# Kernel tuning notes

Hardware: AMD Instinct MI355X
Metric: run time of the kernel (lower is better)

The kernel has to match this reference:

```python
import jax, jax.numpy as jnp
import numpy as np

B, S, D, H = 2, 2048, 1024, 16
DK = D // H


def setup_inputs() -> dict:
    key = jax.random.key(0)
    ks = jax.random.split(key, 12)
    s = 1.0 / np.sqrt(D)
    return {
        "query": jax.random.normal(ks[0], (B, S, D), dtype=jnp.float32),
        "key": jax.random.normal(ks[1], (B, S, D), dtype=jnp.float32),
        "value": jax.random.normal(ks[2], (B, S, D), dtype=jnp.float32),
        "mask": jax.random.randint(ks[3], (B, 1, 1, S), 0, 2, dtype=jnp.int32),
        "wq": jax.random.normal(ks[4], (D, D), dtype=jnp.float32) * s,
        "bq": jnp.zeros((D,), dtype=jnp.float32),
        "wk": jax.random.normal(ks[5], (D, D), dtype=jnp.float32) * s,
        "bk": jnp.zeros((D,), dtype=jnp.float32),
        "wv": jax.random.normal(ks[6], (D, D), dtype=jnp.float32) * s,
        "bv": jnp.zeros((D,), dtype=jnp.float32),
        "wo": jax.random.normal(ks[7], (D, D), dtype=jnp.float32) * s,
        "bo": jnp.zeros((D,), dtype=jnp.float32),
    }


def reference(query, key, value, mask, wq, bq, wk, bk, wv, bv, wo, bo):
    b, s, d = query.shape
    # torch Linear: y = x @ W^T + b, then split heads -> [B, H, S, dk]
    def proj(x, w, bias):
        return (x @ w.T + bias).reshape(b, -1, H, DK).transpose(0, 2, 1, 3)

    q = proj(query, wq, bq)
    k = proj(key, wk, bk)
    v = proj(value, wv, bv)

    scores = jnp.einsum("bhqd,bhkd->bhqk", q, k) / jnp.sqrt(jnp.float32(DK))
    scores = jnp.where(mask == 0, jnp.float32(-1e9), scores)
    attn = jax.nn.softmax(scores, axis=-1)  # [B,H,S,S]
    x = jnp.einsum("bhqk,bhkd->bhqd", attn, v)
    x = x.transpose(0, 2, 1, 3).reshape(b, s, d)
    return x @ wo.T + bo
```

## Files before the change

kernel.cpp:

```cpp
#include <hip/hip_runtime.h>
#include <math.h>

#define B_  2
#define S_  2048
#define D_  1024
#define H_  16
#define DK_ 64
#define NT_ (S_ / 64)

typedef unsigned short u16;
typedef unsigned int u32;
typedef __bf16 bf16x8 __attribute__((ext_vector_type(8)));
typedef float f32x4 __attribute__((ext_vector_type(4)));

typedef const __attribute__((address_space(1))) void* gas1_t;
typedef __attribute__((address_space(3))) void* las3_t;

__device__ __forceinline__ void gload_lds16(const void* g, void* l) {
    __builtin_amdgcn_global_load_lds((gas1_t)g, (las3_t)l, 16, 0, 0);
}

__device__ __forceinline__ u16 f2bf(float f) {
    union { float f; unsigned u; } v; v.f = f;
    return (u16)((v.u + 0x7fffu + ((v.u >> 16) & 1u)) >> 16);
}

__device__ __forceinline__ u32 pack_bf16_2(float lo, float hi) {
    union { float f; u32 u; } a, b;
    a.f = lo; b.f = hi;
    return __builtin_amdgcn_perm(b.u + 0x8000u, a.u + 0x8000u, 0x07060302u);
}

__global__ __launch_bounds__(256)
void cast_all(const float* __restrict__ q, const float* __restrict__ k,
              const float* __restrict__ v, const float* __restrict__ wq,
              const float* __restrict__ wk, const float* __restrict__ wv,
              const float* __restrict__ wo, const int* __restrict__ mask,
              u16* __restrict__ qb, u16* __restrict__ kb, u16* __restrict__ vb,
              u16* __restrict__ wqb, u16* __restrict__ wkb, u16* __restrict__ wvb,
              u16* __restrict__ wob, float* __restrict__ mfac,
              float* __restrict__ nmaskf)
{
    const int bi = blockIdx.x;
    const int tid = threadIdx.x;
    if (bi >= 16400) {
        const int b = bi - 16400;
        __shared__ int red[256];
        int c = 0;
#pragma unroll
        for (int j = 0; j < 8; ++j)
            c += (mask[b * S_ + tid * 8 + j] == 0) ? 1 : 0;
        red[tid] = c;
        __syncthreads();
        for (int s = 128; s > 0; s >>= 1) {
            if (tid < s) red[tid] += red[tid + s];
            __syncthreads();
        }
        if (tid == 0) nmaskf[b] = (float)red[0];
        return;
    }
    if (bi >= 16384) {
        const int idx = (bi - 16384) * 256 + tid;
        mfac[idx] = mask[idx] ? 1.0f : 0.0f;
        return;
    }
    const int i = bi * 256 + tid;
    const float* src; u16* dst; int off;
    if (i < 3 * 1048576) {
        const int seg = i >> 20; off = i & 1048575;
        src = (seg == 0) ? q : (seg == 1) ? k : v;
        dst = (seg == 0) ? qb : (seg == 1) ? kb : vb;
    } else {
        const int j = i - 3 * 1048576;
        const int seg = j >> 18; off = j & 262143;
        src = (seg == 0) ? wq : (seg == 1) ? wk : (seg == 2) ? wv : wo;
        dst = (seg == 0) ? wqb : (seg == 1) ? wkb : (seg == 2) ? wvb : wob;
    }
    const float4 val = ((const float4*)src)[off];
    uint2 o;
    o.x = pack_bf16_2(val.x, val.y);
    o.y = pack_bf16_2(val.z, val.w);
    ((uint2*)dst)[off] = o;
}

template<int BN>
__device__ __forceinline__ void gemm_body(
    const u16* __restrict__ A, const u16* __restrict__ W,
    const float* __restrict__ bias, void* __restrict__ outp,
    float scale, int mode, int m0, int n0,
    const float* __restrict__ rowfac, const float* __restrict__ colfac)
{
    constexpr int NJ = BN / 32;
    __shared__ u16 sA[128 * 64];
    __shared__ u16 sW[BN * 64];

    const int tid  = threadIdx.x;
    const int wave = tid >> 6, lane = tid & 63;
    const int quad = lane >> 4, l16 = lane & 15;
    const int wm = (wave >> 1) * 64;
    const int wn = (wave & 1) * (BN / 2);
    const int srow = lane >> 3;
    const int scol = ((lane & 7) ^ srow) * 8;
    const int sw7  = l16 & 7;

    f32x4 acc[4][NJ];
    const f32x4 zero = {0.f, 0.f, 0.f, 0.f};
#pragma unroll
    for (int i = 0; i < 4; ++i)
#pragma unroll
        for (int j = 0; j < NJ; ++j) acc[i][j] = zero;

    const u16* ast = A + (size_t)(m0 + wave * 8 + srow) * D_ + scol;
    const u16* wst = W + (size_t)(n0 + wave * 8 + srow) * D_ + scol;

    for (int k0 = 0; k0 < D_; k0 += 64) {
#pragma unroll
        for (int t = 0; t < 4; ++t)
            gload_lds16(ast + (size_t)t * 32 * D_ + k0, sA + (wave + t * 4) * 512);
        if (BN == 128) {
#pragma unroll
            for (int t = 0; t < 4; ++t)
                gload_lds16(wst + (size_t)t * 32 * D_ + k0, sW + (wave + t * 4) * 512);
        } else {
#pragma unroll
            for (int t = 0; t < 2; ++t)
                gload_lds16(wst + (size_t)t * 32 * D_ + k0, sW + (wave + t * 4) * 512);
        }
        __syncthreads();

#pragma unroll
        for (int kh = 0; kh < 2; ++kh) {
            const int phys = ((kh * 4 + quad) ^ sw7) * 8;
            bf16x8 af[4], bfr[NJ];
#pragma unroll
            for (int i = 0; i < 4; ++i)
                af[i] = *(const bf16x8*)(sA + (wm + i * 16 + l16) * 64 + phys);
#pragma unroll
            for (int j = 0; j < NJ; ++j)
                bfr[j] = *(const bf16x8*)(sW + (wn + j * 16 + l16) * 64 + phys);
#pragma unroll
            for (int i = 0; i < 4; ++i)
#pragma unroll
                for (int j = 0; j < NJ; ++j)
                    acc[i][j] = __builtin_amdgcn_mfma_f32_16x16x32_bf16(af[i], bfr[j], acc[i][j], 0, 0, 0);
        }
        __syncthreads();
    }

#pragma unroll
    for (int i = 0; i < 4; ++i) {
        float rf4[4];
        if (mode == 1 && rowfac) {
#pragma unroll
            for (int r = 0; r < 4; ++r)
                rf4[r] = rowfac[m0 + wm + i * 16 + quad * 4 + r];
        }
#pragma unroll
        for (int j = 0; j < NJ; ++j) {
            const int n = n0 + wn + j * 16 + l16;
            if (mode == 3) {
                const float cf = colfac ? colfac[n] : 1.0f;
#pragma unroll
                for (int r = 0; r < 4; ++r) {
                    const int mp = m0 + wm + i * 16 + quad * 4 + r;
                    ((u16*)outp)[(size_t)mp * (B_ * S_) + n] = f2bf((acc[i][j][r] + bias[mp]) * cf);
                }
            } else {
                const float bn = bias[n];
#pragma unroll
                for (int r = 0; r < 4; ++r) {
                    const int m = m0 + wm + i * 16 + quad * 4 + r;
                    float v = acc[i][j][r] + bn;
                    if (mode == 0) {
                        ((float*)outp)[(size_t)m * D_ + n] = v;
                    } else {
                        v *= scale;
                        if (rowfac) v *= rf4[r];
                        const int b = m >> 11, s = m & (S_ - 1);
                        const int h = n >> 6, dk = n & 63;
                        ((u16*)outp)[(((size_t)(b * H_ + h)) * S_ + s) * DK_ + dk] = f2bf(v);
                    }
                }
            }
        }
    }
}

__global__ __launch_bounds__(256)
void qkv_gemm(const u16* __restrict__ qin, const u16* __restrict__ kin, const u16* __restrict__ vin,
              const u16* __restrict__ wqb, const u16* __restrict__ wkb, const u16* __restrict__ wvb,
              const float* __restrict__ bq, const float* __restrict__ bk, const float* __restrict__ bv,
              u16* __restrict__ Qp, u16* __restrict__ Kp, u16* __restrict__ Vt,
              const float* __restrict__ mfac)
{
    const int z = blockIdx.z;
    if (z == 2) {
        gemm_body<128>(wvb, vin, bv, Vt, 1.0f, 3, blockIdx.x * 128, blockIdx.y * 128,
                       nullptr, mfac);
    } else {
        const u16* A = (z == 0) ? qin : kin;
        const u16* W = (z == 0) ? wqb : wkb;
        const float* bias = (z == 0) ? bq : bk;
        u16* outp = (z == 0) ? Qp : Kp;
        const float scale = (z == 0) ? 0.18033688011112042f : 1.0f;
        const float* rf = (z == 1) ? mfac : nullptr;
        gemm_body<128>(A, W, bias, outp, scale, 1, blockIdx.y * 128, blockIdx.x * 128,
                       rf, nullptr);
    }
}

__global__ __launch_bounds__(256)
void out_gemm(const u16* __restrict__ Xc, const u16* __restrict__ wob,
              const float* __restrict__ bo, float* __restrict__ out)
{
    gemm_body<64>(Xc, wob, bo, out, 1.0f, 0, blockIdx.y * 128, blockIdx.x * 64,
                  nullptr, nullptr);
}

__global__ __launch_bounds__(256)
void attn_mfma(const u16* __restrict__ Qp, const u16* __restrict__ Kp,
               const u16* __restrict__ Vt, const float* __restrict__ nmaskf,
               u16* __restrict__ Xc)
{
    __shared__ u16 sQ[128 * 64];
    __shared__ u16 sK[2][64 * 64];
    __shared__ u16 sV[2][64 * 64];

    const int tid  = threadIdx.x;
    const int wave = tid >> 6, lane = tid & 63;
    const int quad = lane >> 4, l16 = lane & 15;
    const int qt = blockIdx.x & 15;
    const int bh = blockIdx.x >> 4;
    const int b  = bh >> 4;
    const int h  = bh & 15;
    const int srow = lane >> 3;
    const int scol = ((lane & 7) ^ srow) * 8;
    const int sw7  = l16 & 7;

    const u16* Qb = Qp + ((size_t)bh * S_ + qt * 128) * DK_;
    const u16* Kb = Kp + (size_t)bh * S_ * DK_;
    const u16* Vb = Vt + ((size_t)h * 64) * (B_ * S_) + b * S_;

#pragma unroll
    for (int t = 0; t < 4; ++t)
        gload_lds16(Qb + (size_t)((wave + t * 4) * 8 + srow) * DK_ + scol,
                    sQ + (wave + t * 4) * 512);
#pragma unroll
    for (int t = 0; t < 2; ++t) {
        const int tt = wave + t * 4;
        gload_lds16(Kb + (size_t)(tt * 8 + srow) * DK_ + scol, &sK[0][tt * 512]);
        gload_lds16(Vb + (size_t)(tt * 8 + srow) * (B_ * S_) + scol, &sV[0][tt * 512]);
    }
    __syncthreads();

    bf16x8 qf[2][2];
#pragma unroll
    for (int iq = 0; iq < 2; ++iq)
#pragma unroll
        for (int ks = 0; ks < 2; ++ks) {
            const int row = wave * 32 + iq * 16 + l16;
            const int phys = (ks * 4 + quad) ^ sw7;
            qf[iq][ks] = *(const bf16x8*)(sQ + row * 64 + phys * 8);
        }
    u16* sPw = sQ + wave * 2048;

    bf16x8 vones;
#pragma unroll
    for (int j = 0; j < 8; ++j) vones[j] = (__bf16)1.0f;

    f32x4 oacc[2][4];
    const f32x4 zero = {0.f, 0.f, 0.f, 0.f};
#pragma unroll
    for (int im = 0; im < 2; ++im)
#pragma unroll
        for (int nd = 0; nd < 4; ++nd) oacc[im][nd] = zero;
    f32x4 lfrag[2] = {zero, zero};

    const u16* kpre = Kb + (size_t)64 * DK_ + (size_t)(wave * 8 + srow) * DK_ + scol;
    const u16* vpre = Vb + 64 + (size_t)(wave * 8 + srow) * (B_ * S_) + scol;

    for (int kt = 0; kt < NT_; ++kt) {
        __syncthreads();
        const int cur = kt & 1;

        if (kt < NT_ - 1) {
            u16* kdst = &sK[cur ^ 1][wave * 512];
            u16* vdst = &sV[cur ^ 1][wave * 512];
            gload_lds16(kpre, kdst);
            gload_lds16(kpre + (size_t)32 * DK_, kdst + 4 * 512);
            gload_lds16(vpre, vdst);
            gload_lds16(vpre + (size_t)32 * (B_ * S_), vdst + 4 * 512);
            kpre += (size_t)64 * DK_;
            vpre += 64;
        }

        f32x4 sfr[2][4];
#pragma unroll
        for (int in = 0; in < 4; ++in) {
            const int p0 = (quad ^ sw7) * 8;
            const int p1 = ((4 + quad) ^ sw7) * 8;
            const bf16x8 kf0 = *(const bf16x8*)(&sK[cur][(in * 16 + l16) * 64 + p0]);
            const bf16x8 kf1 = *(const bf16x8*)(&sK[cur][(in * 16 + l16) * 64 + p1]);
#pragma unroll
            for (int iq = 0; iq < 2; ++iq) {
                f32x4 t = __builtin_amdgcn_mfma_f32_16x16x32_bf16(kf0, qf[iq][0], zero, 0, 0, 0);
                sfr[iq][in] = __builtin_amdgcn_mfma_f32_16x16x32_bf16(kf1, qf[iq][1], t, 0, 0, 0);
            }
        }

#pragma unroll
        for (int iq = 0; iq < 2; ++iq) {
#pragma unroll
            for (int in = 0; in < 4; ++in) {
                const float p0 = __builtin_amdgcn_exp2f(sfr[iq][in][0]);
                const float p1 = __builtin_amdgcn_exp2f(sfr[iq][in][1]);
                const float p2 = __builtin_amdgcn_exp2f(sfr[iq][in][2]);
                const float p3 = __builtin_amdgcn_exp2f(sfr[iq][in][3]);
                uint2 o;
                o.x = pack_bf16_2(p0, p1);
                o.y = pack_bf16_2(p2, p3);
                const int pchunk = (in * 2 + (quad >> 1)) ^ sw7;
                *(uint2*)(sPw + (iq * 16 + l16) * 64 + pchunk * 8 + (quad & 1) * 4) = o;
            }
        }

#pragma unroll
        for (int ks = 0; ks < 2; ++ks) {
            const int phys = ((ks * 4 + quad) ^ sw7) * 8;
            bf16x8 pf[2];
#pragma unroll
            for (int im = 0; im < 2; ++im)
                pf[im] = *(const bf16x8*)(sPw + (im * 16 + l16) * 64 + phys);
#pragma unroll
            for (int im = 0; im < 2; ++im)
                lfrag[im] = __builtin_amdgcn_mfma_f32_16x16x32_bf16(pf[im], vones, lfrag[im], 0, 0, 0);
#pragma unroll
            for (int nd = 0; nd < 4; ++nd) {
                const bf16x8 vf = *(const bf16x8*)(&sV[cur][(nd * 16 + l16) * 64 + phys]);
#pragma unroll
                for (int im = 0; im < 2; ++im)
                    oacc[im][nd] = __builtin_amdgcn_mfma_f32_16x16x32_bf16(pf[im], vf, oacc[im][nd], 0, 0, 0);
            }
        }
    }

    const float nm = nmaskf[b];
    float linv[2][4];
#pragma unroll
    for (int im = 0; im < 2; ++im)
#pragma unroll
        for (int r = 0; r < 4; ++r)
            linv[im][r] = __builtin_amdgcn_rcpf(lfrag[im][r] - nm);

#pragma unroll
    for (int im = 0; im < 2; ++im)
#pragma unroll
        for (int r = 0; r < 4; ++r) {
            const int s = qt * 128 + wave * 32 + im * 16 + quad * 4 + r;
            const float inv = linv[im][r];
#pragma unroll
            for (int nd = 0; nd < 4; ++nd)
                Xc[((size_t)(b * S_ + s)) * D_ + h * 64 + nd * 16 + l16] =
                    f2bf(oacc[im][nd][r] * inv);
        }
}

extern "C" void kernel_launch(void* const* d_in, const int* in_sizes, int n_in,
                              void* d_out, int out_size, void* d_ws, size_t ws_size,
                              hipStream_t stream)
{
    (void)in_sizes; (void)n_in; (void)out_size; (void)ws_size;

    const float* query = (const float*)d_in[0];
    const float* key   = (const float*)d_in[1];
    const float* value = (const float*)d_in[2];
    const int*   mask  = (const int*)d_in[3];
    const float* wq    = (const float*)d_in[4];
    const float* bq    = (const float*)d_in[5];
    const float* wk    = (const float*)d_in[6];
    const float* bk    = (const float*)d_in[7];
    const float* wv    = (const float*)d_in[8];
    const float* bv    = (const float*)d_in[9];
    const float* wo    = (const float*)d_in[10];
    const float* bo    = (const float*)d_in[11];

    const size_t NE = (size_t)B_ * S_ * D_;
    const size_t WE = (size_t)D_ * D_;

    u16* qb  = (u16*)d_ws;
    u16* kb  = qb + NE;
    u16* vb  = kb + NE;
    u16* wqb = vb + NE;
    u16* wkb = wqb + WE;
    u16* wvb = wkb + WE;
    u16* wob = wvb + WE;
    u16* Qp  = wob + WE;
    u16* Kp  = Qp + NE;
    u16* Vt  = Kp + NE;
    float* mfac   = (float*)(Vt + NE);
    float* nmaskf = mfac + 4096;
    u16* Xc  = qb;

    cast_all<<<16402, 256, 0, stream>>>(query, key, value, wq, wk, wv, wo, mask,
                                        qb, kb, vb, wqb, wkb, wvb, wob, mfac, nmaskf);

    qkv_gemm<<<dim3(D_ / 128, (B_ * S_) / 128, 3), 256, 0, stream>>>(
        qb, kb, vb, wqb, wkb, wvb, bq, bk, bv, Qp, Kp, Vt, mfac);

    attn_mfma<<<dim3(B_ * H_ * (S_ / 128)), 256, 0, stream>>>(Qp, Kp, Vt, nmaskf, Xc);

    out_gemm<<<dim3(D_ / 64, (B_ * S_) / 128), 256, 0, stream>>>(Xc, wob, bo, (float*)d_out);
}
```

Measured before the change: 237.2 us.

## Split attention KV loop across two wave groups with LDS reduction

The attention kernel now runs 512 threads per block: four query-row wave groups, each doubled across two KV groups that take alternating 32-key tiles and run their own double-buffered loads. At the end, the second KV group writes its partial output accumulators and row sums to LDS, and the first group combines them, normalises and stores. The aim is more waves per block to hide latency, with the 512-block grid being small relative to the CU count. The cost is an extra LDS reduction, smaller MFMA tiles per iteration and tighter register limits from launch_bounds(512,4).

```diff
diff --git a/kernel.cpp b/kernel.cpp
--- a/kernel.cpp
+++ b/kernel.cpp
@@ -6,7 +6,6 @@
 #define D_  1024
 #define H_  16
 #define DK_ 64
-#define NT_ (S_ / 64)
 
 typedef unsigned short u16;
 typedef unsigned int u32;
@@ -217,40 +216,38 @@
                   nullptr, nullptr);
 }
 
-__global__ __launch_bounds__(256)
+__global__ __launch_bounds__(512, 4)
 void attn_mfma(const u16* __restrict__ Qp, const u16* __restrict__ Kp,
                const u16* __restrict__ Vt, const float* __restrict__ nmaskf,
                u16* __restrict__ Xc)
 {
-    __shared__ u16 sQ[128 * 64];
-    __shared__ u16 sK[2][64 * 64];
-    __shared__ u16 sV[2][64 * 64];
+    __shared__ u16 sPQ[8192];
+    __shared__ u16 sKVraw[16384];
 
     const int tid  = threadIdx.x;
     const int wave = tid >> 6, lane = tid & 63;
+    const int qg = wave & 3, kg = wave >> 2;
     const int quad = lane >> 4, l16 = lane & 15;
     const int qt = blockIdx.x & 15;
     const int bh = blockIdx.x >> 4;
     const int b  = bh >> 4;
     const int h  = bh & 15;
-    const int srow = lane >> 3;
-    const int scol = ((lane & 7) ^ srow) * 8;
-    const int sw7  = l16 & 7;
+    const int lr  = lane >> 3;
+    const int cl  = (lane & 7) ^ lr;
+    const int sw7 = l16 & 7;
 
     const u16* Qb = Qp + ((size_t)bh * S_ + qt * 128) * DK_;
     const u16* Kb = Kp + (size_t)bh * S_ * DK_;
-    const u16* Vb = Vt + ((size_t)h * 64) * (B_ * S_) + b * S_;
-
-#pragma unroll
-    for (int t = 0; t < 4; ++t)
-        gload_lds16(Qb + (size_t)((wave + t * 4) * 8 + srow) * DK_ + scol,
-                    sQ + (wave + t * 4) * 512);
-#pragma unroll
-    for (int t = 0; t < 2; ++t) {
-        const int tt = wave + t * 4;
-        gload_lds16(Kb + (size_t)(tt * 8 + srow) * DK_ + scol, &sK[0][tt * 512]);
-        gload_lds16(Vb + (size_t)(tt * 8 + srow) * (B_ * S_) + scol, &sV[0][tt * 512]);
-    }
+    const int vdk = (qg * 8 + lr) + 32 * (cl >> 2);
+    const u16* Vsrc = Vt + (size_t)(h * 64 + vdk) * (B_ * S_) + b * S_ + (cl & 3) * 8;
+    const u16* Ksrc = Kb + (size_t)(qg * 8 + lr) * DK_ + cl * 8;
+
+#pragma unroll
+    for (int t = 0; t < 2; ++t)
+        gload_lds16(Qb + (size_t)(wave * 16 + t * 8 + lr) * DK_ + cl * 8,
+                    sPQ + (wave * 2 + t) * 512);
+    gload_lds16(Ksrc + (size_t)kg * 32 * DK_, sKVraw + (kg * 2) * 4096 + qg * 512);
+    gload_lds16(Vsrc + kg * 32, sKVraw + (kg * 2) * 4096 + 2048 + qg * 512);
     __syncthreads();
 
     bf16x8 qf[2][2];
@@ -258,11 +255,11 @@
     for (int iq = 0; iq < 2; ++iq)
 #pragma unroll
         for (int ks = 0; ks < 2; ++ks) {
-            const int row = wave * 32 + iq * 16 + l16;
-            const int phys = (ks * 4 + quad) ^ sw7;
-            qf[iq][ks] = *(const bf16x8*)(sQ + row * 64 + phys * 8);
-        }
-    u16* sPw = sQ + wave * 2048;
+            const int row = qg * 32 + iq * 16 + l16;
+            const int c = (ks * 4 + quad) ^ sw7;
+            qf[iq][ks] = *(const bf16x8*)(sPQ + row * 64 + c * 8);
+        }
+    u16* sPw = sPQ + wave * 1024;
 
     bf16x8 vones;
 #pragma unroll
@@ -276,31 +273,30 @@
         for (int nd = 0; nd < 4; ++nd) oacc[im][nd] = zero;
     f32x4 lfrag[2] = {zero, zero};
 
-    const u16* kpre = Kb + (size_t)64 * DK_ + (size_t)(wave * 8 + srow) * DK_ + scol;
-    const u16* vpre = Vb + 64 + (size_t)(wave * 8 + srow) * (B_ * S_) + scol;
-
-    for (int kt = 0; kt < NT_; ++kt) {
+    const u16* kpre = Ksrc + (size_t)(kg + 2) * 32 * DK_;
+    const u16* vpre = Vsrc + (kg + 2) * 32;
+
+    for (int i = 0; i < 32; ++i) {
         __syncthreads();
-        const int cur = kt & 1;
-
-        if (kt < NT_ - 1) {
-            u16* kdst = &sK[cur ^ 1][wave * 512];
-            u16* vdst = &sV[cur ^ 1][wave * 512];
-            gload_lds16(kpre, kdst);
-            gload_lds16(kpre + (size_t)32 * DK_, kdst + 4 * 512);
-            gload_lds16(vpre, vdst);
-            gload_lds16(vpre + (size_t)32 * (B_ * S_), vdst + 4 * 512);
-            kpre += (size_t)64 * DK_;
+        const int cur = i & 1;
+
+        if (i < 31) {
+            u16* dst = sKVraw + (kg * 2 + (cur ^ 1)) * 4096;
+            gload_lds16(kpre, dst + qg * 512);
+            gload_lds16(vpre, dst + 2048 + qg * 512);
+            kpre += (size_t)2 * 32 * DK_;
             vpre += 64;
         }
-
-        f32x4 sfr[2][4];
-#pragma unroll
-        for (int in = 0; in < 4; ++in) {
+        const u16* sK = sKVraw + (kg * 2 + cur) * 4096;
+        const u16* sV = sK + 2048;
+
+        f32x4 sfr[2][2];
+#pragma unroll
+        for (int in = 0; in < 2; ++in) {
             const int p0 = (quad ^ sw7) * 8;
             const int p1 = ((4 + quad) ^ sw7) * 8;
-            const bf16x8 kf0 = *(const bf16x8*)(&sK[cur][(in * 16 + l16) * 64 + p0]);
-            const bf16x8 kf1 = *(const bf16x8*)(&sK[cur][(in * 16 + l16) * 64 + p1]);
+            const bf16x8 kf0 = *(const bf16x8*)(sK + (in * 16 + l16) * 64 + p0);
+            const bf16x8 kf1 = *(const bf16x8*)(sK + (in * 16 + l16) * 64 + p1);
 #pragma unroll
             for (int iq = 0; iq < 2; ++iq) {
                 f32x4 t = __builtin_amdgcn_mfma_f32_16x16x32_bf16(kf0, qf[iq][0], zero, 0, 0, 0);
@@ -309,9 +305,9 @@
         }
 
 #pragma unroll
-        for (int iq = 0; iq < 2; ++iq) {
-#pragma unroll
-            for (int in = 0; in < 4; ++in) {
+        for (int iq = 0; iq < 2; ++iq)
+#pragma unroll
+            for (int in = 0; in < 2; ++in) {
                 const float p0 = __builtin_amdgcn_exp2f(sfr[iq][in][0]);
                 const float p1 = __builtin_amdgcn_exp2f(sfr[iq][in][1]);
                 const float p2 = __builtin_amdgcn_exp2f(sfr[iq][in][2]);
@@ -319,50 +315,71 @@
                 uint2 o;
                 o.x = pack_bf16_2(p0, p1);
                 o.y = pack_bf16_2(p2, p3);
-                const int pchunk = (in * 2 + (quad >> 1)) ^ sw7;
-                *(uint2*)(sPw + (iq * 16 + l16) * 64 + pchunk * 8 + (quad & 1) * 4) = o;
-            }
-        }
-
-#pragma unroll
-        for (int ks = 0; ks < 2; ++ks) {
-            const int phys = ((ks * 4 + quad) ^ sw7) * 8;
-            bf16x8 pf[2];
+                const int c = ((in * 2 + (quad >> 1)) + 4 * iq) ^ sw7;
+                *(uint2*)(sPw + l16 * 64 + c * 8 + (quad & 1) * 4) = o;
+            }
+
+        bf16x8 pf[2];
+#pragma unroll
+        for (int im = 0; im < 2; ++im) {
+            const int c = (quad + 4 * im) ^ sw7;
+            pf[im] = *(const bf16x8*)(sPw + l16 * 64 + c * 8);
+            lfrag[im] = __builtin_amdgcn_mfma_f32_16x16x32_bf16(pf[im], vones, lfrag[im], 0, 0, 0);
+        }
+#pragma unroll
+        for (int nd = 0; nd < 4; ++nd) {
+            const int prow = (nd & 1) * 16 + l16;
+            const int vc = (quad + 4 * (nd >> 1)) ^ sw7;
+            const bf16x8 vf = *(const bf16x8*)(sV + prow * 64 + vc * 8);
 #pragma unroll
             for (int im = 0; im < 2; ++im)
-                pf[im] = *(const bf16x8*)(sPw + (im * 16 + l16) * 64 + phys);
-#pragma unroll
-            for (int im = 0; im < 2; ++im)
-                lfrag[im] = __builtin_amdgcn_mfma_f32_16x16x32_bf16(pf[im], vones, lfrag[im], 0, 0, 0);
+                oacc[im][nd] = __builtin_amdgcn_mfma_f32_16x16x32_bf16(pf[im], vf, oacc[im][nd], 0, 0, 0);
+        }
+    }
+
+    __syncthreads();
+    float* sO = (float*)sKVraw;
+    float* sL = (float*)sPQ;
+    if (kg == 1) {
+#pragma unroll
+        for (int im = 0; im < 2; ++im) {
 #pragma unroll
             for (int nd = 0; nd < 4; ++nd) {
-                const bf16x8 vf = *(const bf16x8*)(&sV[cur][(nd * 16 + l16) * 64 + phys]);
-#pragma unroll
-                for (int im = 0; im < 2; ++im)
-                    oacc[im][nd] = __builtin_amdgcn_mfma_f32_16x16x32_bf16(pf[im], vf, oacc[im][nd], 0, 0, 0);
-            }
-        }
-    }
-
-    const float nm = nmaskf[b];
-    float linv[2][4];
-#pragma unroll
-    for (int im = 0; im < 2; ++im)
-#pragma unroll
-        for (int r = 0; r < 4; ++r)
-            linv[im][r] = __builtin_amdgcn_rcpf(lfrag[im][r] - nm);
-
-#pragma unroll
-    for (int im = 0; im < 2; ++im)
-#pragma unroll
-        for (int r = 0; r < 4; ++r) {
-            const int s = qt * 128 + wave * 32 + im * 16 + quad * 4 + r;
-            const float inv = linv[im][r];
-#pragma unroll
-            for (int nd = 0; nd < 4; ++nd)
-                Xc[((size_t)(b * S_ + s)) * D_ + h * 64 + nd * 16 + l16] =
-                    f2bf(oacc[im][nd][r] * inv);
-        }
+                const int col = nd * 16 + l16;
+                const int c = (im * 4 + quad) ^ sw7;
+                *(f32x4*)((char*)(sO + qg * 2048) + col * 128 + c * 16) = oacc[im][nd];
+            }
+            if (l16 == 0) {
+#pragma unroll
+                for (int r = 0; r < 4; ++r)
+                    sL[qg * 32 + im * 16 + quad * 4 + r] = lfrag[im][r];
+            }
+        }
+    }
+    __syncthreads();
+    if (kg == 0) {
+        const float nm = nmaskf[b];
+#pragma unroll
+        for (int im = 0; im < 2; ++im) {
+            float linv[4];
+#pragma unroll
+            for (int r = 0; r < 4; ++r)
+                linv[r] = __builtin_amdgcn_rcpf(
+                    lfrag[im][r] + sL[qg * 32 + im * 16 + quad * 4 + r] - nm);
+#pragma unroll
+            for (int nd = 0; nd < 4; ++nd) {
+                const int col = nd * 16 + l16;
+                const int c = (im * 4 + quad) ^ sw7;
+                const f32x4 o2 = *(const f32x4*)((const char*)(sO + qg * 2048) + col * 128 + c * 16);
+#pragma unroll
+                for (int r = 0; r < 4; ++r) {
+                    const int s = qt * 128 + qg * 32 + im * 16 + quad * 4 + r;
+                    Xc[((size_t)(b * S_ + s)) * D_ + h * 64 + col] =
+                        f2bf((oacc[im][nd][r] + o2[r]) * linv[r]);
+                }
+            }
+        }
+    }
 }
 
 extern "C" void kernel_launch(void* const* d_in, const int* in_sizes, int n_in,
@@ -407,7 +424,7 @@
     qkv_gemm<<<dim3(D_ / 128, (B_ * S_) / 128, 3), 256, 0, stream>>>(
         qb, kb, vb, wqb, wkb, wvb, bq, bk, bv, Qp, Kp, Vt, mfac);
 
-    attn_mfma<<<dim3(B_ * H_ * (S_ / 128)), 256, 0, stream>>>(Qp, Kp, Vt, nmaskf, Xc);
+    attn_mfma<<<dim3(B_ * H_ * (S_ / 128)), 512, 0, stream>>>(Qp, Kp, Vt, nmaskf, Xc);
 
     out_gemm<<<dim3(D_ / 64, (B_ * S_) / 128), 256, 0, stream>>>(Xc, wob, bo, (float*)d_out);
 }
```

After: 226.9 us. 1.05x faster.
